# Performance work log

Hardware: AMD Instinct MI355X
Metric: run time of the kernel (lower is better)

## Reference

```python
import jax, jax.numpy as jnp
import numpy as np

MODEL_DIM = 2048
Q_HEADS = 32
KV_HEADS = 8
HEAD_DIM = MODEL_DIM // Q_HEADS  # 64
ROPE_BASE = 10000.0


def apply_rope(x, pos):
    # x: [B, S, H, D], interleaved-pair RoPE (torchtune-style)
    half = x.shape[-1] // 2
    inv_freq = 1.0 / (ROPE_BASE ** (jnp.arange(half, dtype=jnp.float32) * 2.0 / x.shape[-1]))
    ang = pos.astype(jnp.float32)[:, None] * inv_freq[None, :]        # [S, half]
    cos = jnp.cos(ang)[None, :, None, :]                              # [1,S,1,half]
    sin = jnp.sin(ang)[None, :, None, :]
    x1 = x[..., 0::2]
    x2 = x[..., 1::2]
    o1 = x1 * cos - x2 * sin
    o2 = x2 * cos + x1 * sin
    return jnp.stack([o1, o2], axis=-1).reshape(x.shape)


def setup_inputs() -> dict:
    key = jax.random.key(0)
    ks = jax.random.split(key, 5)
    B, S, D = 2, 2048, MODEL_DIM
    sd = 1.0 / np.sqrt(D)
    x = jax.random.normal(ks[0], (B, S, D), dtype=jnp.float32)
    wq = jax.random.normal(ks[1], (Q_HEADS * HEAD_DIM, D), dtype=jnp.float32) * sd
    wk = jax.random.normal(ks[2], (KV_HEADS * HEAD_DIM, D), dtype=jnp.float32) * sd
    wv = jax.random.normal(ks[3], (KV_HEADS * HEAD_DIM, D), dtype=jnp.float32) * sd
    wo = jax.random.normal(ks[4], (D, D), dtype=jnp.float32) * sd
    attention_mask = jnp.ones((B, S), dtype=bool)
    return {"x": x, "attention_mask": attention_mask, "wq": wq, "wk": wk, "wv": wv, "wo": wo}


def reference(x, attention_mask, wq, wk, wv, wo):
    B, S, D = x.shape
    rep = Q_HEADS // KV_HEADS
    q = (x @ wq.T).reshape(B, S, Q_HEADS, HEAD_DIM)
    k = (x @ wk.T).reshape(B, S, KV_HEADS, HEAD_DIM)
    v = (x @ wv.T).reshape(B, S, KV_HEADS, HEAD_DIM)
    # GQA repeat_interleave along head axis
    k = jnp.repeat(k, rep, axis=2)
    v = jnp.repeat(v, rep, axis=2)
    pos = jnp.arange(S)
    q = apply_rope(q, pos)
    k = apply_rope(k, pos)
    # scores [B, H, Sq, Sk]
    score = jnp.einsum('bqhd,bkhd->bhqk', q, k) / np.sqrt(HEAD_DIM)
    neg_inf = jnp.finfo(score.dtype).min
    causal = jnp.tril(jnp.ones((S, S), dtype=bool))
    score = jnp.where(causal[None, None, :, :], score, neg_inf)
    score = jnp.where(attention_mask[:, None, None, :], score, neg_inf)
    attn = jax.nn.softmax(score, axis=-1)
    out = jnp.einsum('bhqk,bkhd->bqhd', attn, v).reshape(B, S, D)
    return out @ wo.T
```

## Files before the change

### kernel.cpp

```cpp
#include <hip/hip_runtime.h>
#include <hip/hip_bf16.h>

#define S_LEN 2048
#define BATCH 2
#define DMODEL 2048
#define HQ 32
#define HKV 8
#define HD 64
#define NQ 2560
#define KDIM 2048

typedef __attribute__((ext_vector_type(8))) short bf16x8;
typedef __attribute__((ext_vector_type(4))) float f32x4;

#if __has_builtin(__builtin_amdgcn_exp2f)
#define EXP2(x) __builtin_amdgcn_exp2f(x)
#else
#define EXP2(x) exp2f(x)
#endif

static __device__ inline ushort f2bf(float f) {
    union { float f; unsigned u; } v; v.f = f;
    unsigned r = v.u + 0x7fff + ((v.u >> 16) & 1);
    return (ushort)(r >> 16);
}
static __device__ inline float bf2f(ushort h) {
    union { unsigned u; float f; } v; v.u = ((unsigned)h) << 16; return v.f;
}
static __device__ inline unsigned pack2(float lo, float hi) {
    return (unsigned)f2bf(lo) | ((unsigned)f2bf(hi) << 16);
}
static __device__ __forceinline__ unsigned pkbf(float lo, float hi) {
    union { float f; unsigned u; } a, b; a.f = lo; b.f = hi;
    return __builtin_amdgcn_perm(b.u + 0x8000u, a.u + 0x8000u, 0x07060302u);
}

static __device__ __forceinline__ void gload16(const ushort* g, ushort* l) {
    __builtin_amdgcn_global_load_lds(
        (const __attribute__((address_space(1))) unsigned int*)(g),
        (__attribute__((address_space(3))) unsigned int*)(l), 16, 0, 0);
}

#define BARRIER() asm volatile("s_barrier" ::: "memory")
#define WAITVM(N) asm volatile("s_waitcnt vmcnt(" #N ")" ::: "memory")

__global__ __launch_bounds__(256) void convert_kernel(const float* __restrict__ x,
                                                      const float* __restrict__ wq,
                                                      const float* __restrict__ wk,
                                                      const float* __restrict__ wv,
                                                      const float* __restrict__ wo,
                                                      ushort* __restrict__ xb,
                                                      ushort* __restrict__ wqkvb,
                                                      ushort* __restrict__ wob)
{
    size_t e = ((size_t)blockIdx.x * 256 + threadIdx.x) * 8;
    const float* src; ushort* dst;
    if (e < 8388608ul)       { src = x  + e;              dst = xb + e; }
    else if (e < 12582912ul) { src = wq + (e - 8388608);  dst = wqkvb + (e - 8388608); }
    else if (e < 13631488ul) { src = wk + (e - 12582912); dst = wqkvb + 4194304 + (e - 12582912); }
    else if (e < 14680064ul) { src = wv + (e - 13631488); dst = wqkvb + 5242880 + (e - 13631488); }
    else                     { src = wo + (e - 14680064); dst = wob + (e - 14680064); }
    float4 a = *(const float4*)src;
    float4 b = *(const float4*)(src + 4);
    uint4 p; p.x = pack2(a.x, a.y); p.y = pack2(a.z, a.w);
             p.z = pack2(b.x, b.y); p.w = pack2(b.z, b.w);
    *(uint4*)dst = p;
}

template<int NTX, int EPI>
__global__ __launch_bounds__(512, 2) void gemm256(const ushort* __restrict__ A,
                                                  const ushort* __restrict__ Bw,
                                                  ushort* __restrict__ qkv,
                                                  ushort* __restrict__ vT,
                                                  float* __restrict__ Cf)
{
    __shared__ ushort As[2][256 * 64];
    __shared__ ushort Bs[2][256 * 64];
    const int t    = threadIdx.x;
    const int w    = t >> 6, lane = t & 63;
    const int quad = lane >> 4, l15 = lane & 15;
    const int l8   = lane >> 3;
    const int scw  = ((lane & 7) ^ (l8 & 7)) * 8;
    const int wm   = (w >> 2) * 128;
    const int wn   = (w & 3) * 64;

    const int nwg = NTX * 16;
    int bid = blockIdx.x;
    int sb  = (bid & 7) * (nwg >> 3) + (bid >> 3);
    const int mb = (sb / NTX) * 256;
    const int nb = (sb % NTX) * 256;

    f32x4 acc[8][4] = {};
    bf16x8 a[4][2], b0[2][2], b1[2][2];

    auto SA = [&](int buf, int half, int kb) {
        #pragma unroll
        for (int L = 0; L < 2; L++) {
            int r0 = half * 128 + (w * 2 + L) * 8;
            gload16(A + (size_t)(mb + r0 + l8) * KDIM + kb + scw, &As[buf][r0 * 64]);
        }
    };
    auto SB = [&](int buf, int half, int kb) {
        #pragma unroll
        for (int L = 0; L < 2; L++) {
            int r0 = half * 128 + (w * 2 + L) * 8;
            gload16(Bw + (size_t)(nb + r0 + l8) * KDIM + kb + scw, &Bs[buf][r0 * 64]);
        }
    };
    auto LA = [&](int buf, int hm) {
        #pragma unroll
        for (int i = 0; i < 4; i++) {
            int r = wm + hm * 64 + i * 16 + l15;
            int rs = r * 64, sw = r & 7;
            #pragma unroll
            for (int kc = 0; kc < 2; kc++)
                a[i][kc] = *(const bf16x8*)&As[buf][rs + (((kc << 2) | quad) ^ sw) * 8];
        }
    };
    auto LB = [&](int buf, int hn, bf16x8 (&b)[2][2]) {
        #pragma unroll
        for (int j = 0; j < 2; j++) {
            int r = wn + hn * 32 + j * 16 + l15;
            int rs = r * 64, sw = r & 7;
            #pragma unroll
            for (int kc = 0; kc < 2; kc++)
                b[j][kc] = *(const bf16x8*)&Bs[buf][rs + (((kc << 2) | quad) ^ sw) * 8];
        }
    };
    auto MM = [&](bf16x8 (&b)[2][2], int hm, int hn) {
        __builtin_amdgcn_s_setprio(1);
        #pragma unroll
        for (int i = 0; i < 4; i++)
            #pragma unroll
            for (int j = 0; j < 2; j++) {
                f32x4 d = acc[hm * 4 + i][hn * 2 + j];
                d = __builtin_amdgcn_mfma_f32_16x16x32_bf16(a[i][0], b[j][0], d, 0, 0, 0);
                d = __builtin_amdgcn_mfma_f32_16x16x32_bf16(a[i][1], b[j][1], d, 0, 0, 0);
                acc[hm * 4 + i][hn * 2 + j] = d;
            }
        __builtin_amdgcn_s_setprio(0);
    };

    SA(0, 0, 0);  SA(0, 1, 0);  SB(0, 0, 0);  SB(0, 1, 0);
    SA(1, 0, 64); SA(1, 1, 64); SB(1, 0, 64); SB(1, 1, 64);
    WAITVM(8);
    BARRIER();

    #pragma unroll 1
    for (int it = 0; it < 16; it++) {
        const int kb2 = it * 128 + 128;
        const bool pre = (it < 15);
        LA(0, 0); LB(0, 0, b0);
        BARRIER();
        MM(b0, 0, 0);
        BARRIER();
        LB(0, 1, b1);
        BARRIER();
        MM(b1, 0, 1);
        BARRIER();
        LA(0, 1);
        if (pre) { SB(0, 0, kb2); SB(0, 1, kb2); }
        BARRIER();
        MM(b1, 1, 1);
        BARRIER();
        if (pre) { SA(0, 0, kb2); SA(0, 1, kb2); }
        BARRIER();
        MM(b0, 1, 0);
        if (pre) { WAITVM(8); } else { WAITVM(0); }
        BARRIER();
        LA(1, 0); LB(1, 0, b0);
        BARRIER();
        MM(b0, 0, 0);
        BARRIER();
        LB(1, 1, b1);
        BARRIER();
        MM(b1, 0, 1);
        BARRIER();
        LA(1, 1);
        if (pre) { SB(1, 0, kb2 + 64); SB(1, 1, kb2 + 64); }
        BARRIER();
        MM(b1, 1, 1);
        BARRIER();
        if (pre) { SA(1, 0, kb2 + 64); SA(1, 1, kb2 + 64); }
        BARRIER();
        MM(b0, 1, 0);
        if (pre) { WAITVM(8); } else { WAITVM(0); }
        BARRIER();
    }

    #pragma unroll
    for (int i = 0; i < 8; i++) {
        int m0 = mb + wm + (i >> 2) * 64 + (i & 3) * 16 + quad * 4;
        #pragma unroll
        for (int j = 0; j < 4; j++) {
            int n0 = nb + wn + (j >> 1) * 32 + (j & 1) * 16;
            if (EPI == 0) {
                if (n0 >= 2560) {
                    ushort4 pk;
                    pk.x = f2bf(acc[i][j][0]); pk.y = f2bf(acc[i][j][1]);
                    pk.z = f2bf(acc[i][j][2]); pk.w = f2bf(acc[i][j][3]);
                    *(ushort4*)&vT[(size_t)(n0 + l15 - 2560) * 4096 + m0] = pk;
                } else {
                    #pragma unroll
                    for (int r = 0; r < 4; r++)
                        qkv[(size_t)(m0 + r) * NQ + n0 + l15] = f2bf(acc[i][j][r]);
                }
            } else {
                #pragma unroll
                for (int r = 0; r < 4; r++)
                    Cf[(size_t)(m0 + r) * DMODEL + n0 + l15] = acc[i][j][r];
            }
        }
    }
}

__global__ __launch_bounds__(256) void rope_kernel(ushort* __restrict__ qkv)
{
    const int PAIRS = BATCH * S_LEN * (HQ + HKV) * (HD / 2);
    int tid = blockIdx.x * 256 + threadIdx.x;
    if (tid >= PAIRS) return;
    int token = tid / ((HQ + HKV) * 32);
    int r     = tid - token * ((HQ + HKV) * 32);
    int hh    = r >> 5;
    int i     = r & 31;
    int base  = (hh < HQ) ? hh * 64 : DMODEL + (hh - HQ) * 64;
    size_t addr = (size_t)token * NQ + base + 2 * i;
    int s = token & (S_LEN - 1);
    float freq = exp2f(-0.41524101186092f * (float)i);
    float ang  = (float)s * freq;
    float sn, cs;
    sincosf(ang, &sn, &cs);
    float x1 = bf2f(qkv[addr]);
    float x2 = bf2f(qkv[addr + 1]);
    qkv[addr]     = f2bf(x1 * cs - x2 * sn);
    qkv[addr + 1] = f2bf(x2 * cs + x1 * sn);
}

__global__ __launch_bounds__(256) void attn_kernel(const ushort* __restrict__ qkv,
                                                   const ushort* __restrict__ vT,
                                                   ushort* __restrict__ attnb)
{
    __shared__ ushort Ks[2][64 * 64];
    __shared__ ushort VT[2][64 * 64];
    __shared__ ushort PT[4][32 * 72];
    const int t    = threadIdx.x;
    const int w    = t >> 6, lane = t & 63;
    const int quad = lane >> 4, l15 = lane & 15;
    const int bid  = blockIdx.x;
    const int qx   = 15 - (bid >> 6);
    const int h    = bid & 31;
    const int b    = (bid >> 5) & 1;
    const int qb   = qx * 128;
    const int kvh  = h >> 2;
    const ushort* base = qkv + (size_t)b * S_LEN * NQ;
    const ushort* vTb  = vT + (size_t)kvh * HD * 4096 + b * S_LEN;

    const float SC = 0.18033688011112042f;
    bf16x8 aq[2][2];
    #pragma unroll
    for (int h2 = 0; h2 < 2; h2++) {
        const ushort* qp = base + (size_t)(qb + w * 32 + h2 * 16 + l15) * NQ + h * HD + quad * 8;
        #pragma unroll
        for (int hf = 0; hf < 2; hf++) {
            bf16x8 v = *(const bf16x8*)(qp + hf * 32);
            #pragma unroll
            for (int j = 0; j < 8; j++) v[j] = (short)f2bf(bf2f((ushort)v[j]) * SC);
            aq[h2][hf] = v;
        }
    }

    f32x4 o[2][4] = {};
    float lsum[2] = {};
    const int qw    = qb + w * 32;
    const int strow = lane >> 3;
    const int stlc  = (lane & 7) ^ strow;
    ushort* ptw = &PT[w][0];
    const int niter = (qb + 128) / 64;

    #pragma unroll
    for (int c = 0; c < 2; c++) {
        int key = w * 16 + c * 8 + strow;
        gload16(base + (size_t)key * NQ + DMODEL + kvh * HD + stlc * 8,
                &Ks[0][(w * 16 + c * 8) * 64]);
        gload16(vTb + (size_t)key * 4096 + stlc * 8,
                &VT[0][(w * 16 + c * 8) * 64]);
    }

    for (int i = 0; i < niter; i++) {
        const int kb  = i * 64;
        const int cur = i & 1;
        __syncthreads();
        if (i + 1 < niter) {
            int kb2 = kb + 64;
            #pragma unroll
            for (int c = 0; c < 2; c++) {
                int key = w * 16 + c * 8 + strow;
                gload16(base + (size_t)(kb2 + key) * NQ + DMODEL + kvh * HD + stlc * 8,
                        &Ks[1 - cur][(w * 16 + c * 8) * 64]);
                gload16(vTb + (size_t)key * 4096 + kb2 + stlc * 8,
                        &VT[1 - cur][(w * 16 + c * 8) * 64]);
            }
        }
        if (kb <= qw + 31) {
            const bool full = (kb + 63) <= qw;
            const ushort* ks = &Ks[cur][0];
            const ushort* vs = &VT[cur][0];
            f32x4 s[2][4];
            #pragma unroll
            for (int kt = 0; kt < 4; kt++) {
                int key = kt * 16 + l15;
                int sw  = l15 & 7;
                bf16x8 k0 = *(const bf16x8*)&ks[key * 64 + (quad ^ sw) * 8];
                bf16x8 k1 = *(const bf16x8*)&ks[key * 64 + (((quad + 4) & 7) ^ sw) * 8];
                #pragma unroll
                for (int h2 = 0; h2 < 2; h2++) {
                    f32x4 z = {};
                    z = __builtin_amdgcn_mfma_f32_16x16x32_bf16(k0, aq[h2][0], z, 0, 0, 0);
                    z = __builtin_amdgcn_mfma_f32_16x16x32_bf16(k1, aq[h2][1], z, 0, 0, 0);
                    s[h2][kt] = z;
                }
            }
            #pragma unroll
            for (int h2 = 0; h2 < 2; h2++) {
                int rq    = h2 * 16 + l15;
                int wbase = rq * 72 + (quad & 1) * 4;
                #pragma unroll
                for (int kt = 0; kt < 4; kt++) {
                    float p0 = EXP2(s[h2][kt][0]);
                    float p1 = EXP2(s[h2][kt][1]);
                    float p2 = EXP2(s[h2][kt][2]);
                    float p3 = EXP2(s[h2][kt][3]);
                    if (!full) {
                        int key0 = kb + kt * 16 + quad * 4;
                        int q    = qb + w * 32 + rq;
                        p0 = (key0 + 0 <= q) ? p0 : 0.f;
                        p1 = (key0 + 1 <= q) ? p1 : 0.f;
                        p2 = (key0 + 2 <= q) ? p2 : 0.f;
                        p3 = (key0 + 3 <= q) ? p3 : 0.f;
                    }
                    lsum[h2] += (p0 + p1) + (p2 + p3);
                    int pc = kt * 2 + (quad >> 1);
                    uint2 pk;
                    pk.x = pkbf(p0, p1);
                    pk.y = pkbf(p2, p3);
                    *(uint2*)&ptw[wbase + pc * 8] = pk;
                }
            }
            bf16x8 pf[2][2];
            #pragma unroll
            for (int h2 = 0; h2 < 2; h2++) {
                int rq = h2 * 16 + l15;
                #pragma unroll
                for (int kc = 0; kc < 2; kc++)
                    pf[h2][kc] = *(const bf16x8*)&ptw[rq * 72 + (kc * 4 + quad) * 8];
            }
            #pragma unroll
            for (int tt = 0; tt < 4; tt++) {
                int dr = tt * 16 + l15;
                int sw = l15 & 7;
                bf16x8 vf0 = *(const bf16x8*)&vs[dr * 64 + (quad ^ sw) * 8];
                bf16x8 vf1 = *(const bf16x8*)&vs[dr * 64 + (((quad + 4) & 7) ^ sw) * 8];
                #pragma unroll
                for (int h2 = 0; h2 < 2; h2++) {
                    f32x4 oo = o[h2][tt];
                    oo = __builtin_amdgcn_mfma_f32_16x16x32_bf16(vf0, pf[h2][0], oo, 0, 0, 0);
                    oo = __builtin_amdgcn_mfma_f32_16x16x32_bf16(vf1, pf[h2][1], oo, 0, 0, 0);
                    o[h2][tt] = oo;
                }
            }
        }
    }
    #pragma unroll
    for (int h2 = 0; h2 < 2; h2++) {
        float l = lsum[h2];
        l += __shfl_xor(l, 16, 64);
        l += __shfl_xor(l, 32, 64);
        float inv = 1.0f / l;
        ushort* ob = attnb + (size_t)(b * S_LEN + qb + w * 32 + h2 * 16 + l15) * DMODEL
                   + h * HD + quad * 4;
        #pragma unroll
        for (int tt = 0; tt < 4; tt++) {
            uint2 st;
            st.x = pkbf(o[h2][tt][0] * inv, o[h2][tt][1] * inv);
            st.y = pkbf(o[h2][tt][2] * inv, o[h2][tt][3] * inv);
            *(uint2*)&ob[tt * 16] = st;
        }
    }
}

extern "C" void kernel_launch(void* const* d_in, const int* in_sizes, int n_in,
                              void* d_out, int out_size, void* d_ws, size_t ws_size,
                              hipStream_t stream)
{
    const float* x  = (const float*)d_in[0];
    const float* wq = (const float*)d_in[2];
    const float* wk = (const float*)d_in[3];
    const float* wv = (const float*)d_in[4];
    const float* wo = (const float*)d_in[5];
    float* out = (float*)d_out;

    char* ws = (char*)d_ws;
    ushort* qkv    = (ushort*)(ws);
    ushort* vT     = (ushort*)(ws + 20971520);
    ushort* xb     = (ushort*)(ws + 25165824);
    ushort* attn_b = xb;
    ushort* wqkvb  = (ushort*)(ws + 41943040);
    ushort* wob    = (ushort*)(ws + 54525952);

    convert_kernel<<<9216, 256, 0, stream>>>(x, wq, wk, wv, wo, xb, wqkvb, wob);

    gemm256<12, 0><<<192, 512, 0, stream>>>(xb, wqkvb, qkv, vT, nullptr);

    int pairs = BATCH * S_LEN * (HQ + HKV) * (HD / 2);
    rope_kernel<<<(pairs + 255) / 256, 256, 0, stream>>>(qkv);

    attn_kernel<<<1024, 256, 0, stream>>>(qkv, vT, attn_b);

    gemm256<8, 1><<<128, 512, 0, stream>>>(attn_b, wob, nullptr, nullptr, out);
}
```

Before: 307.1 us.

## Shrink GEMM N-tile to fill all CUs and restructure K-loop pipeline

The GEMM tile changes from 256x256 to 256xBN, with BN=192 for the QKV projection and BN=128 for the output projection, so both GEMMs launch 256 workgroups instead of 192 or 128. The goal is to occupy all CUs of the MI355X rather than leaving many idle. The K loop is rewritten as a single-tile-per-step pipeline that splits A-loads by halves, uses new vmcnt waits and needs an explicit epilogue. The cost is less operand reuse per tile, plus tight coupling between the pipeline and the hand-computed wait counts.

```diff
diff --git a/kernel.cpp b/kernel.cpp
--- a/kernel.cpp
+++ b/kernel.cpp
@@ -18,6 +18,8 @@
 #else
 #define EXP2(x) exp2f(x)
 #endif
+
+template<int N> struct ic { static constexpr int value = N; };
 
 static __device__ inline ushort f2bf(float f) {
     union { float f; unsigned u; } v; v.f = f;
@@ -67,43 +69,44 @@
     *(uint4*)dst = p;
 }
 
-template<int NTX, int EPI>
+template<int BNF, int EPI>
 __global__ __launch_bounds__(512, 2) void gemm256(const ushort* __restrict__ A,
                                                   const ushort* __restrict__ Bw,
                                                   ushort* __restrict__ qkv,
                                                   ushort* __restrict__ vT,
                                                   float* __restrict__ Cf)
 {
+    constexpr int BN = BNF * 64;
+    constexpr int KT = KDIM / 64;
     __shared__ ushort As[2][256 * 64];
-    __shared__ ushort Bs[2][256 * 64];
+    __shared__ ushort Bs[2][BN * 64];
     const int t    = threadIdx.x;
     const int w    = t >> 6, lane = t & 63;
     const int quad = lane >> 4, l15 = lane & 15;
     const int l8   = lane >> 3;
     const int scw  = ((lane & 7) ^ (l8 & 7)) * 8;
     const int wm   = (w >> 2) * 128;
-    const int wn   = (w & 3) * 64;
-
-    const int nwg = NTX * 16;
-    int bid = blockIdx.x;
-    int sb  = (bid & 7) * (nwg >> 3) + (bid >> 3);
-    const int mb = (sb / NTX) * 256;
-    const int nb = (sb % NTX) * 256;
-
-    f32x4 acc[8][4] = {};
-    bf16x8 a[4][2], b0[2][2], b1[2][2];
-
-    auto SA = [&](int buf, int half, int kb) {
+    const int wn   = (w & 3) * (BNF * 16);
+
+    const int bid = blockIdx.x;
+    const int sb  = (bid & 7) * 32 + (bid >> 3);
+    const int mb  = (sb >> 4) * 256;
+    const int nb  = (sb & 15) * BN;
+
+    f32x4 acc[8][BNF] = {};
+    bf16x8 a[4][2], b[BNF][2];
+
+    auto SAH = [&](int buf, int half, int kb) {
         #pragma unroll
         for (int L = 0; L < 2; L++) {
             int r0 = half * 128 + (w * 2 + L) * 8;
             gload16(A + (size_t)(mb + r0 + l8) * KDIM + kb + scw, &As[buf][r0 * 64]);
         }
     };
-    auto SB = [&](int buf, int half, int kb) {
-        #pragma unroll
-        for (int L = 0; L < 2; L++) {
-            int r0 = half * 128 + (w * 2 + L) * 8;
+    auto SB = [&](int buf, int kb) {
+        #pragma unroll
+        for (int L = 0; L < BNF; L++) {
+            int r0 = (w * BNF + L) * 8;
             gload16(Bw + (size_t)(nb + r0 + l8) * KDIM + kb + scw, &Bs[buf][r0 * 64]);
         }
     };
@@ -117,83 +120,78 @@
                 a[i][kc] = *(const bf16x8*)&As[buf][rs + (((kc << 2) | quad) ^ sw) * 8];
         }
     };
-    auto LB = [&](int buf, int hn, bf16x8 (&b)[2][2]) {
-        #pragma unroll
-        for (int j = 0; j < 2; j++) {
-            int r = wn + hn * 32 + j * 16 + l15;
+    auto LB = [&](int buf) {
+        #pragma unroll
+        for (int j = 0; j < BNF; j++) {
+            int r = wn + j * 16 + l15;
             int rs = r * 64, sw = r & 7;
             #pragma unroll
             for (int kc = 0; kc < 2; kc++)
                 b[j][kc] = *(const bf16x8*)&Bs[buf][rs + (((kc << 2) | quad) ^ sw) * 8];
         }
     };
-    auto MM = [&](bf16x8 (&b)[2][2], int hm, int hn) {
+    auto MM = [&](auto HM) {
+        constexpr int hm = decltype(HM)::value;
         __builtin_amdgcn_s_setprio(1);
         #pragma unroll
         for (int i = 0; i < 4; i++)
             #pragma unroll
-            for (int j = 0; j < 2; j++) {
-                f32x4 d = acc[hm * 4 + i][hn * 2 + j];
+            for (int j = 0; j < BNF; j++) {
+                f32x4 d = acc[hm * 4 + i][j];
                 d = __builtin_amdgcn_mfma_f32_16x16x32_bf16(a[i][0], b[j][0], d, 0, 0, 0);
                 d = __builtin_amdgcn_mfma_f32_16x16x32_bf16(a[i][1], b[j][1], d, 0, 0, 0);
-                acc[hm * 4 + i][hn * 2 + j] = d;
+                acc[hm * 4 + i][j] = d;
             }
         __builtin_amdgcn_s_setprio(0);
     };
 
-    SA(0, 0, 0);  SA(0, 1, 0);  SB(0, 0, 0);  SB(0, 1, 0);
-    SA(1, 0, 64); SA(1, 1, 64); SB(1, 0, 64); SB(1, 1, 64);
-    WAITVM(8);
+    SAH(0, 0, 0); SAH(0, 1, 0); SB(0, 0);
+    SAH(1, 0, 64); SB(1, 64);
+    if constexpr (BNF == 3) WAITVM(5); else WAITVM(4);
     BARRIER();
 
     #pragma unroll 1
-    for (int it = 0; it < 16; it++) {
-        const int kb2 = it * 128 + 128;
-        const bool pre = (it < 15);
-        LA(0, 0); LB(0, 0, b0);
+    for (int tt = 0; tt < KT - 2; tt++) {
+        const int buf = tt & 1, o = buf ^ 1;
+        LA(buf, 0); LB(buf);
+        SAH(o, 1, (tt + 1) * 64);
         BARRIER();
-        MM(b0, 0, 0);
+        MM(ic<0>{});
+        if constexpr (BNF == 3) WAITVM(7); else WAITVM(6);
         BARRIER();
-        LB(0, 1, b1);
+        LA(buf, 1);
+        SAH(buf, 0, (tt + 2) * 64); SB(buf, (tt + 2) * 64);
         BARRIER();
-        MM(b1, 0, 1);
+        MM(ic<1>{});
+        if constexpr (BNF == 3) WAITVM(7); else WAITVM(6);
         BARRIER();
-        LA(0, 1);
-        if (pre) { SB(0, 0, kb2); SB(0, 1, kb2); }
-        BARRIER();
-        MM(b1, 1, 1);
-        BARRIER();
-        if (pre) { SA(0, 0, kb2); SA(0, 1, kb2); }
-        BARRIER();
-        MM(b0, 1, 0);
-        if (pre) { WAITVM(8); } else { WAITVM(0); }
-        BARRIER();
-        LA(1, 0); LB(1, 0, b0);
-        BARRIER();
-        MM(b0, 0, 0);
-        BARRIER();
-        LB(1, 1, b1);
-        BARRIER();
-        MM(b1, 0, 1);
-        BARRIER();
-        LA(1, 1);
-        if (pre) { SB(1, 0, kb2 + 64); SB(1, 1, kb2 + 64); }
-        BARRIER();
-        MM(b1, 1, 1);
-        BARRIER();
-        if (pre) { SA(1, 0, kb2 + 64); SA(1, 1, kb2 + 64); }
-        BARRIER();
-        MM(b0, 1, 0);
-        if (pre) { WAITVM(8); } else { WAITVM(0); }
-        BARRIER();
-    }
+    }
+    LA(0, 0); LB(0);
+    SAH(1, 1, (KT - 1) * 64);
+    BARRIER();
+    MM(ic<0>{});
+    if constexpr (BNF == 3) WAITVM(7); else WAITVM(6);
+    BARRIER();
+    LA(0, 1);
+    BARRIER();
+    MM(ic<1>{});
+    WAITVM(2);
+    BARRIER();
+    LA(1, 0); LB(1);
+    BARRIER();
+    MM(ic<0>{});
+    WAITVM(0);
+    BARRIER();
+    LA(1, 1);
+    BARRIER();
+    MM(ic<1>{});
 
     #pragma unroll
     for (int i = 0; i < 8; i++) {
         int m0 = mb + wm + (i >> 2) * 64 + (i & 3) * 16 + quad * 4;
         #pragma unroll
-        for (int j = 0; j < 4; j++) {
-            int n0 = nb + wn + (j >> 1) * 32 + (j & 1) * 16;
+        for (int j = 0; j < BNF; j++) {
+            int n0 = nb + wn + j * 16;
             if (EPI == 0) {
                 if (n0 >= 2560) {
                     ushort4 pk;
@@ -409,12 +407,12 @@
 
     convert_kernel<<<9216, 256, 0, stream>>>(x, wq, wk, wv, wo, xb, wqkvb, wob);
 
-    gemm256<12, 0><<<192, 512, 0, stream>>>(xb, wqkvb, qkv, vT, nullptr);
+    gemm256<3, 0><<<256, 512, 0, stream>>>(xb, wqkvb, qkv, vT, nullptr);
 
     int pairs = BATCH * S_LEN * (HQ + HKV) * (HD / 2);
     rope_kernel<<<(pairs + 255) / 256, 256, 0, stream>>>(qkv);
 
     attn_kernel<<<1024, 256, 0, stream>>>(qkv, vT, attn_b);
 
-    gemm256<8, 1><<<128, 512, 0, stream>>>(attn_b, wob, nullptr, nullptr, out);
-}
+    gemm256<2, 1><<<256, 512, 0, stream>>>(attn_b, wob, nullptr, nullptr, out);
+}
```

Result: faster. 273.9 us (-10.8%).
